# Kernel tuning notes

Hardware: AMD Instinct MI355X
Metric: run time of the kernel (lower is better)

## Reference

```python
import jax, jax.numpy as jnp
import numpy as np

B, H, NQ, NK, D = 2, 16, 4096, 4096, 64


def _attn_with_lse(q, k, v, scale):
    # q: [B,H,p,d], k: [B,H,s,d], v: [B,H,s,dv]
    s = jnp.einsum('bhqd,bhkd->bhqk', q, k) * scale
    lse = jax.nn.logsumexp(s, axis=-1, keepdims=True)  # [B,H,p,1]
    p = jnp.exp(s - lse)
    o = jnp.einsum('bhqk,bhkd->bhqd', p, v)
    return o, lse


def setup_inputs() -> dict:
    key = jax.random.key(0)
    k1, k2, k3 = jax.random.split(key, 3)
    return {
        'query': jax.random.normal(k1, (B, H, NQ, D), dtype=jnp.float32),
        'key': jax.random.normal(k2, (B, H, NK, D), dtype=jnp.float32),
        'value': jax.random.normal(k3, (B, H, NK, D), dtype=jnp.float32),
        'n_query_groups': 4,
        'n_key_groups': 4,
    }


def reference(query, key, value, n_query_groups, n_key_groups):
    b, h, nq, d = query.shape
    nk = key.shape[2]
    m, n = int(n_query_groups), int(n_key_groups)
    scale = d ** (-0.5)
    pq, pk = nq // m, nk // n  # group sizes n_gp
    c0, c1 = m // 2, n // 2   # center groups c_gp

    # representative query/key blocks
    q_gp = query[:, :, c0 * pq:(c0 + 1) * pq, :]              # [B,H,pq,d]
    k_gp = key[:, :, c1 * pk:(c1 + 1) * pk, :]                # [B,H,pk,d]
    # value chunks concatenated on feature dim (zero-padding of q/k in the
    # original leaves the dot products unchanged, so we skip it)
    v_gp = value.reshape(b, h, n, pk, d).transpose(0, 1, 3, 2, 4).reshape(b, h, pk, n * d)
    attn_gp, lse_gp = _attn_with_lse(q_gp, k_gp, v_gp, scale)  # [B,H,pq,n*d], [B,H,pq,1]

    # sample one key per key group (torch uses random.randint; fixed to 0 here)
    k_picked = 0
    k_sample = key[:, :, k_picked::pk, :]                      # [B,H,n,d]
    w = jnp.einsum('bhqd,bhnd->bhqn', query, k_sample)         # [B,H,nq,n]
    w_gps = w.reshape(b, h, m, pq, n)
    norm_gps = jnp.linalg.norm(w_gps, axis=-2)                 # [B,H,m,n]
    s_gps = norm_gps / norm_gps[:, :, c0, c1][:, :, None, None]

    v_sum = value.reshape(b, h, n, pk, d).sum(axis=3)          # [B,H,n,d]
    om = jnp.maximum(1.0 - s_gps, 0.0)                         # clamp(1-s, min=0)
    num_part1 = om[:, :, :, :, None, None] * v_sum[:, :, None, :, None, :]  # [B,H,m,n,1,d]
    den_part1 = (om * pk)[:, :, :, :, None, None]              # [B,H,m,n,1,1]

    lse_exp = jnp.exp(lse_gp)                                  # [B,H,pq,1]
    unnorm = lse_exp * attn_gp                                 # [B,H,pq,n*d]
    attn_gps = unnorm.reshape(b, h, pq, n, d).transpose(0, 1, 3, 2, 4)  # [B,H,n,pq,d]
    num_part2 = s_gps[:, :, :, :, None, None] * attn_gps[:, :, None, :, :, :]  # [B,H,m,n,pq,d]
    den_part2 = s_gps[:, :, :, :, None, None] * lse_exp[:, :, None, None, :, :]  # [B,H,m,n,pq,1]

    num_agg = (num_part1 + num_part2).sum(axis=3)              # [B,H,m,pq,d]
    den_agg = (den_part1 + den_part2).sum(axis=3)              # [B,H,m,pq,1]

    attn = (num_agg / den_agg).reshape(b, h, nq, d)
    lse = jnp.log(den_agg).reshape(b, h, nq, 1)
    return attn, lse
```

## Files before the change

kernel.cpp:

```cpp
#include <hip/hip_runtime.h>
#include <hip/hip_bf16.h>


#define BH_TOT 32
#define SEQ    4096
#define DIM    64
#define PQ     1024

#define QB_OFF 34816u
#define KB_OFF (QB_OFF + 4u*1024u*1024u)
#define VB_OFF (KB_OFF + 4u*1024u*1024u)
#define WS_NEED (VB_OFF + 16u*1024u*1024u)

#define QSCALE 0.1803368801111204f

typedef __attribute__((ext_vector_type(8))) short bf16x8;
typedef __attribute__((ext_vector_type(4))) short bf16x4;
typedef __attribute__((ext_vector_type(4))) float f32x4;
typedef __attribute__((ext_vector_type(4))) _Float16 f16x4;
typedef __attribute__((ext_vector_type(8))) _Float16 f16x8;

__device__ __forceinline__ short f2bf(float x) {
    unsigned u = __float_as_uint(x);
    u = u + 0x7fffu + ((u >> 16) & 1u);
    return (short)(u >> 16);
}
__device__ __forceinline__ float bf2f(unsigned short h) {
    return __uint_as_float(((unsigned)h) << 16);
}

__global__ __launch_bounds__(256) void mega_prep(
    const float* __restrict__ query, const float* __restrict__ key,
    const float* __restrict__ value, float* __restrict__ ws,
    char* __restrict__ wsb)
{
    __shared__ union {
        struct { float ksm[4][64]; float wsum[4][16]; } n;
        struct { float Ls[64][68]; float ps[4][64]; } v;
    } sm;
    const int t = threadIdx.x;
    const int bid = blockIdx.x;

    if (bid < 512) {
        const int bh = bid >> 4, gi = (bid >> 2) & 3, chunk = bid & 3;
        sm.n.ksm[t >> 6][t & 63] =
            key[((size_t)bh * SEQ + (size_t)(t >> 6) * PQ) * DIM + (t & 63)];
        __syncthreads();
        const int wv = t >> 6, lane = t & 63, c = lane & 15, hi = lane >> 4;
        bf16x8 bb0, bb1;
#pragma unroll
        for (int j = 0; j < 8; ++j) {
            bb0[j] = (c < 4) ? f2bf(sm.n.ksm[c][hi * 8 + j]) : (short)0;
            bb1[j] = (c < 4) ? f2bf(sm.n.ksm[c][32 + hi * 8 + j]) : (short)0;
        }
        float acc0 = 0.f, acc1 = 0.f, acc2 = 0.f, acc3 = 0.f;
        const float* qbase = query +
            ((size_t)bh * SEQ + (size_t)gi * PQ + (size_t)chunk * 256) * DIM;
#pragma unroll
        for (int it = 0; it < 4; ++it) {
            const int row = (wv * 4 + it) * 16 + c;
            const float* qp = qbase + (size_t)row * 64 + hi * 8;
            float4 a0 = *(const float4*)qp;
            float4 a1 = *(const float4*)(qp + 4);
            float4 a2 = *(const float4*)(qp + 32);
            float4 a3 = *(const float4*)(qp + 36);
            bf16x8 qa0, qa1;
            qa0[0] = f2bf(a0.x); qa0[1] = f2bf(a0.y); qa0[2] = f2bf(a0.z); qa0[3] = f2bf(a0.w);
            qa0[4] = f2bf(a1.x); qa0[5] = f2bf(a1.y); qa0[6] = f2bf(a1.z); qa0[7] = f2bf(a1.w);
            qa1[0] = f2bf(a2.x); qa1[1] = f2bf(a2.y); qa1[2] = f2bf(a2.z); qa1[3] = f2bf(a2.w);
            qa1[4] = f2bf(a3.x); qa1[5] = f2bf(a3.y); qa1[6] = f2bf(a3.z); qa1[7] = f2bf(a3.w);
            f32x4 s = (f32x4){0.f, 0.f, 0.f, 0.f};
            s = __builtin_amdgcn_mfma_f32_16x16x32_bf16(qa0, bb0, s, 0, 0, 0);
            s = __builtin_amdgcn_mfma_f32_16x16x32_bf16(qa1, bb1, s, 0, 0, 0);
            acc0 += s[0] * s[0]; acc1 += s[1] * s[1];
            acc2 += s[2] * s[2]; acc3 += s[3] * s[3];
        }
        float asum = acc0 + acc1 + acc2 + acc3;
        asum += __shfl_xor(asum, 16);
        asum += __shfl_xor(asum, 32);
        if (lane < 16) sm.n.wsum[wv][lane] = asum;
        __syncthreads();
        if (t < 4)
            atomicAdd(&ws[bh * 16 + gi * 4 + t],
                      sm.n.wsum[0][t] + sm.n.wsum[1][t] + sm.n.wsum[2][t] + sm.n.wsum[3][t]);
    } else if (bid < 2560) {
        const int blk = bid - 512;
        const int bh = blk >> 6, gj = (blk >> 4) & 3, kc = blk & 15;
        const float* src = value + ((size_t)bh * SEQ + gj * PQ + kc * 64) * DIM;
#pragma unroll
        for (int i = 0; i < 4; ++i) {
            const int u = t + i * 256;
            const int row = u >> 4, c4 = (u & 15) * 4;
            *(float4*)&sm.v.Ls[row][c4] = *(const float4*)(src + row * 64 + c4);
        }
        __syncthreads();
        {
            const int d = t & 63, rg = t >> 6;
            float s = 0.f;
#pragma unroll
            for (int i = 0; i < 16; ++i) s += sm.v.Ls[rg * 16 + i][d];
            sm.v.ps[rg][d] = s;
        }
        __syncthreads();
        if (t < 64) {
            float tot = sm.v.ps[0][t] + sm.v.ps[1][t] + sm.v.ps[2][t] + sm.v.ps[3][t];
            atomicAdd(&ws[512 + bh * 256 + gj * 64 + t], tot);
        }
#pragma unroll
        for (int i = 0; i < 2; ++i) {
            const int sid = t + i * 256;
            const int pl = sid >> 8, dt = (sid >> 6) & 3, lane = sid & 63;
            const int c = lane & 15, hi = lane >> 4;
            f16x8 h;
#pragma unroll
            for (int j = 0; j < 8; ++j)
                h[j] = (_Float16)sm.v.Ls[pl * 32 + hi * 8 + j][dt * 16 + c];
            const size_t off = ((((size_t)(bh * 4 + gj) * 32 + kc * 2 + pl) * 4 + dt) * 64 + lane) * 16;
            *(f16x8*)(wsb + VB_OFF + off) = h;
        }
    } else if (bid < 3072) {
        const int qb = bid - 2560;
        const int bh = qb >> 4, qt = qb & 15;
#pragma unroll
        for (int i = 0; i < 2; ++i) {
            const int sid = t + i * 256;
            const int mt = sid >> 7, kh = (sid >> 6) & 1, lane = sid & 63;
            const int c = lane & 15, hi = lane >> 4;
            const float* p = query + ((size_t)bh * SEQ + 2048 + qt * 64 + mt * 16 + c) * DIM
                             + kh * 32 + hi * 8;
            float4 a = *(const float4*)p, b = *(const float4*)(p + 4);
            bf16x8 h;
            h[0] = f2bf(a.x * QSCALE); h[1] = f2bf(a.y * QSCALE);
            h[2] = f2bf(a.z * QSCALE); h[3] = f2bf(a.w * QSCALE);
            h[4] = f2bf(b.x * QSCALE); h[5] = f2bf(b.y * QSCALE);
            h[6] = f2bf(b.z * QSCALE); h[7] = f2bf(b.w * QSCALE);
            const size_t fidx = ((size_t)(bh * 16 + qt) * 4 + mt) * 2 + kh;
            *(bf16x8*)(wsb + QB_OFF + fidx * 1024 + lane * 16) = h;
        }
    } else {
        const int b2 = bid - 3072;
        const int bh = b2 >> 4, kc = b2 & 15;
#pragma unroll
        for (int i = 0; i < 2; ++i) {
            const int sid = t + i * 256;
            const int kh = sid >> 8, nt = (sid >> 6) & 3, lane = sid & 63;
            const int c = lane & 15, hi = lane >> 4;
            const float* p = key + ((size_t)bh * SEQ + 2048 + kc * 64 + nt * 16 + c) * DIM
                             + kh * 32 + hi * 8;
            float4 a = *(const float4*)p, b = *(const float4*)(p + 4);
            bf16x8 h;
            h[0] = f2bf(a.x); h[1] = f2bf(a.y); h[2] = f2bf(a.z); h[3] = f2bf(a.w);
            h[4] = f2bf(b.x); h[5] = f2bf(b.y); h[6] = f2bf(b.z); h[7] = f2bf(b.w);
            const size_t fidx = ((size_t)(bh * 16 + kc) * 2 + kh) * 4 + nt;
            *(bf16x8*)(wsb + KB_OFF + fidx * 1024 + lane * 16) = h;
        }
    }
}

__global__ __launch_bounds__(256, 4) void kattn4(
    const char* __restrict__ wsb, float* __restrict__ out)
{
    __shared__ union {
        _Float16 Pf[2][2][2][512];
        float Uf[32][257];
    } lds;
    __shared__ float Llds[32];

    const int blk = blockIdx.x;
    const int slot = blk >> 3;
    const int bh = (blk & 7) * 4 + (slot >> 5);
    const int qt = slot & 31;
    const int t = threadIdx.x;
    const int w = t >> 6, lane = t & 63;
    const int c = lane & 15, hi = lane >> 4;

    bf16x8 aq[2][2];
#pragma unroll
    for (int qt2 = 0; qt2 < 2; ++qt2) {
        const int s = qt * 2 + qt2;
        const size_t fr = ((size_t)(bh * 16 + (s >> 2)) * 4 + (s & 3)) * 2;
        aq[qt2][0] = *(const bf16x8*)(wsb + QB_OFF + fr * 1024 + lane * 16);
        aq[qt2][1] = *(const bf16x8*)(wsb + QB_OFF + (fr + 1) * 1024 + lane * 16);
    }
    const char* kb = wsb + KB_OFF + ((size_t)(bh * 16) * 8) * 1024 + (size_t)w * 1024 + lane * 16;
    const char* vb = wsb + VB_OFF + ((size_t)(bh * 4 + w) * 128) * 1024 + lane * 16;

    f32x4 Uacc[2][4];
#pragma unroll
    for (int mt = 0; mt < 2; ++mt)
#pragma unroll
        for (int dt = 0; dt < 4; ++dt)
            Uacc[mt][dt] = (f32x4){0.f, 0.f, 0.f, 0.f};
    f32x4 Lacc[2];
    Lacc[0] = (f32x4){0.f, 0.f, 0.f, 0.f};
    Lacc[1] = (f32x4){0.f, 0.f, 0.f, 0.f};
    f16x8 kOnes;
#pragma unroll
    for (int j = 0; j < 8; ++j) kOnes[j] = (_Float16)1.f;

    const int k0 = w * 16 + hi * 4;
    const int pspan = k0 >> 5;
    const int pidx = (c + 16 * ((k0 & 31) >> 3)) * 8 + (k0 & 7);

    bf16x8 bk0 = *(const bf16x8*)(kb);
    bf16x8 bk1 = *(const bf16x8*)(kb + 4096);

    for (int kc = 0; kc < 16; ++kc) {
        const int buf = kc & 1;
        const char* vcb = vb + (size_t)kc * 8192;
        f16x8 vf[8];
#pragma unroll
        for (int u = 0; u < 8; ++u) vf[u] = *(const f16x8*)(vcb + u * 1024);
        f32x4 sacc[2];
        __builtin_amdgcn_s_setprio(1);
#pragma unroll
        for (int qt2 = 0; qt2 < 2; ++qt2) {
            f32x4 s = (f32x4){0.f, 0.f, 0.f, 0.f};
            s = __builtin_amdgcn_mfma_f32_16x16x32_bf16(bk0, aq[qt2][0], s, 0, 0, 0);
            s = __builtin_amdgcn_mfma_f32_16x16x32_bf16(bk1, aq[qt2][1], s, 0, 0, 0);
            sacc[qt2] = s;
        }
        __builtin_amdgcn_s_setprio(0);
        if (kc < 15) {
            bk0 = *(const bf16x8*)(kb + (size_t)(kc + 1) * 8192);
            bk1 = *(const bf16x8*)(kb + (size_t)(kc + 1) * 8192 + 4096);
        }
#pragma unroll
        for (int qt2 = 0; qt2 < 2; ++qt2) {
            f16x4 ph;
#pragma unroll
            for (int r = 0; r < 4; ++r)
                ph[r] = (_Float16)__builtin_amdgcn_exp2f(sacc[qt2][r]);
            *(f16x4*)&lds.Pf[buf][qt2][pspan][pidx] = ph;
        }
        asm volatile("s_waitcnt lgkmcnt(0)" ::: "memory");
        __builtin_amdgcn_s_barrier();
        f16x8 ap[2][2];
#pragma unroll
        for (int mt = 0; mt < 2; ++mt)
#pragma unroll
            for (int sp = 0; sp < 2; ++sp)
                ap[mt][sp] = *(const f16x8*)&lds.Pf[buf][mt][sp][lane * 8];
        __builtin_amdgcn_s_setprio(1);
#pragma unroll
        for (int mt = 0; mt < 2; ++mt) {
#pragma unroll
            for (int sp = 0; sp < 2; ++sp) {
                Uacc[mt][0] = __builtin_amdgcn_mfma_f32_16x16x32_f16(ap[mt][sp], vf[sp * 4 + 0], Uacc[mt][0], 0, 0, 0);
                Uacc[mt][1] = __builtin_amdgcn_mfma_f32_16x16x32_f16(ap[mt][sp], vf[sp * 4 + 1], Uacc[mt][1], 0, 0, 0);
                Uacc[mt][2] = __builtin_amdgcn_mfma_f32_16x16x32_f16(ap[mt][sp], vf[sp * 4 + 2], Uacc[mt][2], 0, 0, 0);
                Uacc[mt][3] = __builtin_amdgcn_mfma_f32_16x16x32_f16(ap[mt][sp], vf[sp * 4 + 3], Uacc[mt][3], 0, 0, 0);
                Lacc[mt]    = __builtin_amdgcn_mfma_f32_16x16x32_f16(ap[mt][sp], kOnes, Lacc[mt], 0, 0, 0);
            }
        }
        __builtin_amdgcn_s_setprio(0);
    }

    __syncthreads();
#pragma unroll
    for (int mt = 0; mt < 2; ++mt)
#pragma unroll
        for (int dt = 0; dt < 4; ++dt)
#pragma unroll
            for (int r = 0; r < 4; ++r)
                lds.Uf[mt * 16 + hi * 4 + r][w * 64 + dt * 16 + c] = Uacc[mt][dt][r];
    if (w == 0 && c == 0) {
#pragma unroll
        for (int mt = 0; mt < 2; ++mt)
#pragma unroll
            for (int r = 0; r < 4; ++r)
                Llds[mt * 16 + hi * 4 + r] = Lacc[mt][r];
    }
    __syncthreads();

    const float* wsf = (const float*)wsb;
    const float* nsq = wsf + (size_t)bh * 16;
    const float* vsw = wsf + 512 + (size_t)bh * 256;
    const int dd = t & 63, rq = t >> 6;
    float sg[4][4], ssum[4], omp[4], ov[4];
    const float inv22 = 1.0f / nsq[10];
#pragma unroll
    for (int gi = 0; gi < 4; ++gi) {
        float ss = 0.f, os = 0.f, ovv = 0.f;
#pragma unroll
        for (int gj = 0; gj < 4; ++gj) {
            float sgv = sqrtf(nsq[gi * 4 + gj] * inv22);
            sg[gi][gj] = sgv;
            ss += sgv;
            float om = fmaxf(1.0f - sgv, 0.0f);
            os += om;
            ovv += om * vsw[gj * 64 + dd];
        }
        ssum[gi] = ss; omp[gi] = os * 1024.0f; ov[gi] = ovv;
    }
    const size_t base = (size_t)bh * SEQ * DIM;
    float* attn_out = out + base;
    float* lse_out = out + (size_t)BH_TOT * SEQ * DIM + (size_t)bh * SEQ;
    for (int k = 0; k < 8; ++k) {
        const int r = k * 4 + rq;
        const float u0 = lds.Uf[r][dd];
        const float u1 = lds.Uf[r][64 + dd];
        const float u2 = lds.Uf[r][128 + dd];
        const float u3 = lds.Uf[r][192 + dd];
        const float Lr = Llds[r];
        const int orow = qt * 32 + r;
#pragma unroll
        for (int gi = 0; gi < 4; ++gi) {
            float num = ov[gi] + sg[gi][0] * u0 + sg[gi][1] * u1 + sg[gi][2] * u2 + sg[gi][3] * u3;
            float den = omp[gi] + ssum[gi] * Lr;
            attn_out[(size_t)(gi * 1024 + orow) * 64 + dd] = num * __builtin_amdgcn_rcpf(den);
            if (dd == gi) lse_out[gi * 1024 + orow] = __logf(den);
        }
    }
}

__global__ __launch_bounds__(256) void prep_norm2(
    const float* __restrict__ query, const float* __restrict__ key,
    float* __restrict__ ws)
{
    __shared__ float ksm[4][64];
    __shared__ float wsum[4][16];
    const int t = threadIdx.x;
    const int bh = blockIdx.x >> 2, gi = blockIdx.x & 3;
    if (t < 64) ws[512 + blockIdx.x * 64 + t] = 0.f;
    ksm[t >> 6][t & 63] = key[((size_t)bh * SEQ + (size_t)(t >> 6) * PQ) * DIM + (t & 63)];
    __syncthreads();
    const int wv = t >> 6, lane = t & 63, c = lane & 15, hi = lane >> 4;
    bf16x8 bb0, bb1;
#pragma unroll
    for (int j = 0; j < 8; ++j) {
        bb0[j] = (c < 4) ? f2bf(ksm[c][hi * 8 + j]) : (short)0;
        bb1[j] = (c < 4) ? f2bf(ksm[c][32 + hi * 8 + j]) : (short)0;
    }
    float acc0 = 0.f, acc1 = 0.f, acc2 = 0.f, acc3 = 0.f;
    const float* qbase = query + ((size_t)bh * SEQ + (size_t)gi * PQ) * DIM;
    for (int it = 0; it < 16; ++it) {
        const int row = (wv * 16 + it) * 16 + c;
        const float* qp = qbase + (size_t)row * 64 + hi * 8;
        float4 a0 = *(const float4*)qp;
        float4 a1 = *(const float4*)(qp + 4);
        float4 a2 = *(const float4*)(qp + 32);
        float4 a3 = *(const float4*)(qp + 36);
        bf16x8 qa0, qa1;
        qa0[0] = f2bf(a0.x); qa0[1] = f2bf(a0.y); qa0[2] = f2bf(a0.z); qa0[3] = f2bf(a0.w);
        qa0[4] = f2bf(a1.x); qa0[5] = f2bf(a1.y); qa0[6] = f2bf(a1.z); qa0[7] = f2bf(a1.w);
        qa1[0] = f2bf(a2.x); qa1[1] = f2bf(a2.y); qa1[2] = f2bf(a2.z); qa1[3] = f2bf(a2.w);
        qa1[4] = f2bf(a3.x); qa1[5] = f2bf(a3.y); qa1[6] = f2bf(a3.z); qa1[7] = f2bf(a3.w);
        f32x4 s = (f32x4){0.f, 0.f, 0.f, 0.f};
        s = __builtin_amdgcn_mfma_f32_16x16x32_bf16(qa0, bb0, s, 0, 0, 0);
        s = __builtin_amdgcn_mfma_f32_16x16x32_bf16(qa1, bb1, s, 0, 0, 0);
        acc0 += s[0] * s[0]; acc1 += s[1] * s[1];
        acc2 += s[2] * s[2]; acc3 += s[3] * s[3];
    }
    float asum = acc0 + acc1 + acc2 + acc3;
    asum += __shfl_xor(asum, 16);
    asum += __shfl_xor(asum, 32);
    if (lane < 16) wsum[wv][lane] = asum;
    __syncthreads();
    if (t < 4) ws[bh * 16 + gi * 4 + t] = wsum[0][t] + wsum[1][t] + wsum[2][t] + wsum[3][t];
}

__global__ __launch_bounds__(256) void prep_vsum(
    const float* __restrict__ value, float* __restrict__ ws)
{
    __shared__ float part[16][16][4];
    const int t = threadIdx.x;
    const int bh = blockIdx.x >> 2, gj = blockIdx.x & 3;
    const float4* vv = (const float4*)(value + ((size_t)bh * SEQ + (size_t)gj * PQ) * DIM);
    const int c4 = t & 15, rg = t >> 4;
    float a0 = 0.f, a1 = 0.f, a2 = 0.f, a3 = 0.f;
    for (int r = rg; r < 1024; r += 16) {
        float4 x = vv[r * 16 + c4];
        a0 += x.x; a1 += x.y; a2 += x.z; a3 += x.w;
    }
    part[rg][c4][0] = a0; part[rg][c4][1] = a1;
    part[rg][c4][2] = a2; part[rg][c4][3] = a3;
    __syncthreads();
    if (t < 64) {
        const int cc = t >> 2, comp = t & 3;
        float s = 0.f;
#pragma unroll
        for (int g = 0; g < 16; ++g) s += part[g][cc][comp];
        ws[512 + bh * 256 + gj * 64 + cc * 4 + comp] = s;
    }
}

__global__ __launch_bounds__(256, 2) void kattn_fallback(
    const float* __restrict__ query, const float* __restrict__ key,
    const float* __restrict__ value, const float* __restrict__ ws,
    float* __restrict__ out)
{
    __shared__ union {
        struct { short Q[64][72]; short K[64][72]; short P[64][72]; } s;
        unsigned short U[64][264];
    } lds;
    __shared__ float Llds[64];
    const int blk = blockIdx.x;
    const int bh = blk >> 4, qt = blk & 15;
    const int t = threadIdx.x;
    const int w = t >> 6, lane = t & 63;
    const int c = lane & 15, hi = lane >> 4;
    const size_t base = (size_t)bh * SEQ * DIM;
    {
        const float* qp = query + base + (size_t)(2048 + qt * 64) * DIM;
#pragma unroll
        for (int k2 = 0; k2 < 4; ++k2) {
            int u = t + k2 * 256;
            int row = u >> 4, ci = (u & 15) * 4;
            float4 qv = *(const float4*)(qp + row * 64 + ci);
            bf16x4 h;
            h[0] = f2bf(qv.x); h[1] = f2bf(qv.y); h[2] = f2bf(qv.z); h[3] = f2bf(qv.w);
            *(bf16x4*)&lds.s.Q[row][ci] = h;
        }
    }
    __syncthreads();
    bf16x8 aq0 = *(const bf16x8*)&lds.s.Q[w * 16 + c][hi * 8];
    bf16x8 aq1 = *(const bf16x8*)&lds.s.Q[w * 16 + c][32 + hi * 8];
    f32x4 Uacc[4][4];
#pragma unroll
    for (int mt = 0; mt < 4; ++mt)
#pragma unroll
        for (int nt = 0; nt < 4; ++nt)
            Uacc[mt][nt] = (f32x4){0.f, 0.f, 0.f, 0.f};
    float Lacc[4] = {0.f, 0.f, 0.f, 0.f};
    const float* kp = key + base + (size_t)2048 * DIM;
    const float* vgrp = value + base + (size_t)w * PQ * DIM;
    for (int kc = 0; kc < 16; ++kc) {
        {
            const float* kcp = kp + (size_t)kc * 64 * DIM;
#pragma unroll
            for (int k2 = 0; k2 < 4; ++k2) {
                int u = t + k2 * 256;
                int row = u >> 4, ci = (u & 15) * 4;
                float4 kv = *(const float4*)(kcp + row * 64 + ci);
                bf16x4 h;
                h[0] = f2bf(kv.x); h[1] = f2bf(kv.y); h[2] = f2bf(kv.z); h[3] = f2bf(kv.w);
                *(bf16x4*)&lds.s.K[row][ci] = h;
            }
        }
        __syncthreads();
        f32x4 sacc[4];
#pragma unroll
        for (int nt = 0; nt < 4; ++nt) sacc[nt] = (f32x4){0.f, 0.f, 0.f, 0.f};
#pragma unroll
        for (int nt = 0; nt < 4; ++nt) {
            bf16x8 bk = *(const bf16x8*)&lds.s.K[nt * 16 + c][hi * 8];
            sacc[nt] = __builtin_amdgcn_mfma_f32_16x16x32_bf16(aq0, bk, sacc[nt], 0, 0, 0);
        }
#pragma unroll
        for (int nt = 0; nt < 4; ++nt) {
            bf16x8 bk = *(const bf16x8*)&lds.s.K[nt * 16 + c][32 + hi * 8];
            sacc[nt] = __builtin_amdgcn_mfma_f32_16x16x32_bf16(aq1, bk, sacc[nt], 0, 0, 0);
        }
        float p[4][4];
#pragma unroll
        for (int nt = 0; nt < 4; ++nt)
#pragma unroll
            for (int r = 0; r < 4; ++r)
                p[nt][r] = __expf(sacc[nt][r] * 0.125f);
#pragma unroll
        for (int r = 0; r < 4; ++r) {
            float rs = p[0][r] + p[1][r] + p[2][r] + p[3][r];
            rs += __shfl_xor(rs, 1); rs += __shfl_xor(rs, 2);
            rs += __shfl_xor(rs, 4); rs += __shfl_xor(rs, 8);
            Lacc[r] += rs;
        }
#pragma unroll
        for (int nt = 0; nt < 4; ++nt)
#pragma unroll
            for (int r = 0; r < 4; ++r)
                lds.s.P[w * 16 + hi * 4 + r][nt * 16 + c] = (unsigned short)f2bf(p[nt][r]);
        __syncthreads();
        bf16x8 ap2[4][2];
#pragma unroll
        for (int mt = 0; mt < 4; ++mt) {
            ap2[mt][0] = *(const bf16x8*)&lds.s.P[mt * 16 + c][hi * 8];
            ap2[mt][1] = *(const bf16x8*)&lds.s.P[mt * 16 + c][32 + hi * 8];
        }
        const float* vp = vgrp + (size_t)kc * 64 * DIM;
#pragma unroll
        for (int kt = 0; kt < 2; ++kt) {
#pragma unroll
            for (int nt = 0; nt < 4; ++nt) {
                const float* vpp = vp + (kt * 32 + hi * 8) * 64 + nt * 16 + c;
                bf16x8 bv;
#pragma unroll
                for (int j = 0; j < 8; ++j) bv[j] = f2bf(vpp[j * 64]);
#pragma unroll
                for (int mt = 0; mt < 4; ++mt)
                    Uacc[mt][nt] = __builtin_amdgcn_mfma_f32_16x16x32_bf16(ap2[mt][kt], bv, Uacc[mt][nt], 0, 0, 0);
            }
        }
        __syncthreads();
    }
#pragma unroll
    for (int mt = 0; mt < 4; ++mt)
#pragma unroll
        for (int nt = 0; nt < 4; ++nt)
#pragma unroll
            for (int r = 0; r < 4; ++r)
                lds.U[mt * 16 + hi * 4 + r][w * 64 + nt * 16 + c] =
                    (unsigned short)f2bf(Uacc[mt][nt][r]);
    if (c == 0) {
#pragma unroll
        for (int r = 0; r < 4; ++r) Llds[w * 16 + hi * 4 + r] = Lacc[r];
    }
    __syncthreads();
    const float* nsq = ws + bh * 16;
    const float* vsw = ws + 512 + bh * 256;
    const int dd = t & 63, rq = t >> 6;
    float sg[4][4], ssum[4], omp[4], ov[4];
    const float inv22 = 1.0f / nsq[10];
#pragma unroll
    for (int gi = 0; gi < 4; ++gi) {
        float ss = 0.f, os = 0.f, ovv = 0.f;
#pragma unroll
        for (int gj = 0; gj < 4; ++gj) {
            float sgv = sqrtf(nsq[gi * 4 + gj] * inv22);
            sg[gi][gj] = sgv;
            ss += sgv;
            float om = fmaxf(1.0f - sgv, 0.0f);
            os += om;
            ovv += om * vsw[gj * 64 + dd];
        }
        ssum[gi] = ss; omp[gi] = os * 1024.0f; ov[gi] = ovv;
    }
    float* attn_out = out + base;
    float* lse_out = out + (size_t)BH_TOT * SEQ * DIM + (size_t)bh * SEQ;
    for (int k = 0; k < 16; ++k) {
        const int r = k * 4 + rq;
        const float u0 = bf2f(lds.U[r][dd]);
        const float u1 = bf2f(lds.U[r][64 + dd]);
        const float u2 = bf2f(lds.U[r][128 + dd]);
        const float u3 = bf2f(lds.U[r][192 + dd]);
        const float Lr = Llds[r];
        const int orow = qt * 64 + r;
#pragma unroll
        for (int gi = 0; gi < 4; ++gi) {
            float num = ov[gi] + sg[gi][0] * u0 + sg[gi][1] * u1 + sg[gi][2] * u2 + sg[gi][3] * u3;
            float den = omp[gi] + ssum[gi] * Lr;
            attn_out[(size_t)(gi * 1024 + orow) * 64 + dd] = num / den;
            if (dd == gi) lse_out[gi * 1024 + orow] = __logf(den);
        }
    }
}

extern "C" void kernel_launch(void* const* d_in, const int* in_sizes, int n_in,
                              void* d_out, int out_size, void* d_ws, size_t ws_size,
                              hipStream_t stream)
{
    (void)in_sizes; (void)n_in; (void)out_size;
    const float* query = (const float*)d_in[0];
    const float* key   = (const float*)d_in[1];
    const float* value = (const float*)d_in[2];
    float* ws   = (float*)d_ws;
    char*  wsb  = (char*)d_ws;
    float* outp = (float*)d_out;

    if (ws_size >= WS_NEED) {
        (void)hipMemsetAsync(d_ws, 0, QB_OFF, stream);
        mega_prep<<<3584, 256, 0, stream>>>(query, key, value, ws, wsb);
        kattn4<<<1024, 256, 0, stream>>>(wsb, outp);
    } else {
        prep_norm2<<<128, 256, 0, stream>>>(query, key, ws);
        prep_vsum<<<128, 256, 0, stream>>>(value, ws);
        kattn_fallback<<<512, 256, 0, stream>>>(query, key, value, ws, outp);
    }
}
```

Before: 170.8 us.

## Double query rows per attention block and compute prep norms with FP32 dot products

Each attention block now handles 64 query rows instead of 32, so every K/V fragment it loads feeds twice as many MFMAs. Launch bounds drop to 2 blocks per CU and the grid halves. The epilogue now stages U through LDS in 16-row slices to keep LDS usage down, at the cost of extra barriers. The query-norm prep path is also changed from bf16 MFMA to plain FP32 per-thread dot products with wave shuffles and direct atomics, trading matrix-unit work for scalar FMAs and more atomics.

```diff
diff --git a/kernel.cpp b/kernel.cpp
--- a/kernel.cpp
+++ b/kernel.cpp
@@ -35,7 +35,7 @@
     char* __restrict__ wsb)
 {
     __shared__ union {
-        struct { float ksm[4][64]; float wsum[4][16]; } n;
+        struct { float ksm[4][64]; } n;
         struct { float Ls[64][68]; float ps[4][64]; } v;
     } sm;
     const int t = threadIdx.x;
@@ -46,43 +46,36 @@
         sm.n.ksm[t >> 6][t & 63] =
             key[((size_t)bh * SEQ + (size_t)(t >> 6) * PQ) * DIM + (t & 63)];
         __syncthreads();
-        const int wv = t >> 6, lane = t & 63, c = lane & 15, hi = lane >> 4;
-        bf16x8 bb0, bb1;
-#pragma unroll
-        for (int j = 0; j < 8; ++j) {
-            bb0[j] = (c < 4) ? f2bf(sm.n.ksm[c][hi * 8 + j]) : (short)0;
-            bb1[j] = (c < 4) ? f2bf(sm.n.ksm[c][32 + hi * 8 + j]) : (short)0;
-        }
-        float acc0 = 0.f, acc1 = 0.f, acc2 = 0.f, acc3 = 0.f;
-        const float* qbase = query +
-            ((size_t)bh * SEQ + (size_t)gi * PQ + (size_t)chunk * 256) * DIM;
-#pragma unroll
-        for (int it = 0; it < 4; ++it) {
-            const int row = (wv * 4 + it) * 16 + c;
-            const float* qp = qbase + (size_t)row * 64 + hi * 8;
-            float4 a0 = *(const float4*)qp;
-            float4 a1 = *(const float4*)(qp + 4);
-            float4 a2 = *(const float4*)(qp + 32);
-            float4 a3 = *(const float4*)(qp + 36);
-            bf16x8 qa0, qa1;
-            qa0[0] = f2bf(a0.x); qa0[1] = f2bf(a0.y); qa0[2] = f2bf(a0.z); qa0[3] = f2bf(a0.w);
-            qa0[4] = f2bf(a1.x); qa0[5] = f2bf(a1.y); qa0[6] = f2bf(a1.z); qa0[7] = f2bf(a1.w);
-            qa1[0] = f2bf(a2.x); qa1[1] = f2bf(a2.y); qa1[2] = f2bf(a2.z); qa1[3] = f2bf(a2.w);
-            qa1[4] = f2bf(a3.x); qa1[5] = f2bf(a3.y); qa1[6] = f2bf(a3.z); qa1[7] = f2bf(a3.w);
-            f32x4 s = (f32x4){0.f, 0.f, 0.f, 0.f};
-            s = __builtin_amdgcn_mfma_f32_16x16x32_bf16(qa0, bb0, s, 0, 0, 0);
-            s = __builtin_amdgcn_mfma_f32_16x16x32_bf16(qa1, bb1, s, 0, 0, 0);
-            acc0 += s[0] * s[0]; acc1 += s[1] * s[1];
-            acc2 += s[2] * s[2]; acc3 += s[3] * s[3];
-        }
-        float asum = acc0 + acc1 + acc2 + acc3;
-        asum += __shfl_xor(asum, 16);
-        asum += __shfl_xor(asum, 32);
-        if (lane < 16) sm.n.wsum[wv][lane] = asum;
-        __syncthreads();
-        if (t < 4)
-            atomicAdd(&ws[bh * 16 + gi * 4 + t],
-                      sm.n.wsum[0][t] + sm.n.wsum[1][t] + sm.n.wsum[2][t] + sm.n.wsum[3][t]);
+        const int lane = t & 63;
+        const float* qp = query +
+            ((size_t)bh * SEQ + (size_t)gi * PQ + (size_t)chunk * 256 + t) * DIM;
+        float d0 = 0.f, d1 = 0.f, d2 = 0.f, d3 = 0.f;
+#pragma unroll
+        for (int j = 0; j < 16; ++j) {
+            float4 x = *(const float4*)(qp + j * 4);
+            const float* k0 = &sm.n.ksm[0][j * 4];
+            const float* k1 = &sm.n.ksm[1][j * 4];
+            const float* k2 = &sm.n.ksm[2][j * 4];
+            const float* k3 = &sm.n.ksm[3][j * 4];
+            d0 += x.x * k0[0] + x.y * k0[1] + x.z * k0[2] + x.w * k0[3];
+            d1 += x.x * k1[0] + x.y * k1[1] + x.z * k1[2] + x.w * k1[3];
+            d2 += x.x * k2[0] + x.y * k2[1] + x.z * k2[2] + x.w * k2[3];
+            d3 += x.x * k3[0] + x.y * k3[1] + x.z * k3[2] + x.w * k3[3];
+        }
+        float s0 = d0 * d0, s1 = d1 * d1, s2 = d2 * d2, s3 = d3 * d3;
+#pragma unroll
+        for (int off = 1; off < 64; off <<= 1) {
+            s0 += __shfl_xor(s0, off);
+            s1 += __shfl_xor(s1, off);
+            s2 += __shfl_xor(s2, off);
+            s3 += __shfl_xor(s3, off);
+        }
+        if (lane == 0) {
+            atomicAdd(&ws[bh * 16 + gi * 4 + 0], s0);
+            atomicAdd(&ws[bh * 16 + gi * 4 + 1], s1);
+            atomicAdd(&ws[bh * 16 + gi * 4 + 2], s2);
+            atomicAdd(&ws[bh * 16 + gi * 4 + 3], s3);
+        }
     } else if (bid < 2560) {
         const int blk = bid - 512;
         const int bh = blk >> 6, gj = (blk >> 4) & 3, kc = blk & 15;
@@ -157,43 +150,42 @@
     }
 }
 
-__global__ __launch_bounds__(256, 4) void kattn4(
+__global__ __launch_bounds__(256, 2) void kattn4(
     const char* __restrict__ wsb, float* __restrict__ out)
 {
     __shared__ union {
-        _Float16 Pf[2][2][2][512];
-        float Uf[32][257];
+        _Float16 Pf[2][4][2][512];
+        float Uf[16][257];
     } lds;
-    __shared__ float Llds[32];
+    __shared__ float Llds[64];
 
     const int blk = blockIdx.x;
     const int slot = blk >> 3;
-    const int bh = (blk & 7) * 4 + (slot >> 5);
-    const int qt = slot & 31;
+    const int bh = (blk & 7) * 4 + (slot >> 4);
+    const int qt = slot & 15;
     const int t = threadIdx.x;
     const int w = t >> 6, lane = t & 63;
     const int c = lane & 15, hi = lane >> 4;
 
-    bf16x8 aq[2][2];
-#pragma unroll
-    for (int qt2 = 0; qt2 < 2; ++qt2) {
-        const int s = qt * 2 + qt2;
-        const size_t fr = ((size_t)(bh * 16 + (s >> 2)) * 4 + (s & 3)) * 2;
+    bf16x8 aq[4][2];
+#pragma unroll
+    for (int qt2 = 0; qt2 < 4; ++qt2) {
+        const size_t fr = (((size_t)bh * 16 + qt) * 4 + qt2) * 2;
         aq[qt2][0] = *(const bf16x8*)(wsb + QB_OFF + fr * 1024 + lane * 16);
         aq[qt2][1] = *(const bf16x8*)(wsb + QB_OFF + (fr + 1) * 1024 + lane * 16);
     }
     const char* kb = wsb + KB_OFF + ((size_t)(bh * 16) * 8) * 1024 + (size_t)w * 1024 + lane * 16;
     const char* vb = wsb + VB_OFF + ((size_t)(bh * 4 + w) * 128) * 1024 + lane * 16;
 
-    f32x4 Uacc[2][4];
-#pragma unroll
-    for (int mt = 0; mt < 2; ++mt)
+    f32x4 Uacc[4][4];
+#pragma unroll
+    for (int mt = 0; mt < 4; ++mt)
 #pragma unroll
         for (int dt = 0; dt < 4; ++dt)
             Uacc[mt][dt] = (f32x4){0.f, 0.f, 0.f, 0.f};
-    f32x4 Lacc[2];
-    Lacc[0] = (f32x4){0.f, 0.f, 0.f, 0.f};
-    Lacc[1] = (f32x4){0.f, 0.f, 0.f, 0.f};
+    f32x4 Lacc[4];
+#pragma unroll
+    for (int mt = 0; mt < 4; ++mt) Lacc[mt] = (f32x4){0.f, 0.f, 0.f, 0.f};
     f16x8 kOnes;
 #pragma unroll
     for (int j = 0; j < 8; ++j) kOnes[j] = (_Float16)1.f;
@@ -211,10 +203,10 @@
         f16x8 vf[8];
 #pragma unroll
         for (int u = 0; u < 8; ++u) vf[u] = *(const f16x8*)(vcb + u * 1024);
-        f32x4 sacc[2];
+        f32x4 sacc[4];
         __builtin_amdgcn_s_setprio(1);
 #pragma unroll
-        for (int qt2 = 0; qt2 < 2; ++qt2) {
+        for (int qt2 = 0; qt2 < 4; ++qt2) {
             f32x4 s = (f32x4){0.f, 0.f, 0.f, 0.f};
             s = __builtin_amdgcn_mfma_f32_16x16x32_bf16(bk0, aq[qt2][0], s, 0, 0, 0);
             s = __builtin_amdgcn_mfma_f32_16x16x32_bf16(bk1, aq[qt2][1], s, 0, 0, 0);
@@ -226,7 +218,7 @@
             bk1 = *(const bf16x8*)(kb + (size_t)(kc + 1) * 8192 + 4096);
         }
 #pragma unroll
-        for (int qt2 = 0; qt2 < 2; ++qt2) {
+        for (int qt2 = 0; qt2 < 4; ++qt2) {
             f16x4 ph;
 #pragma unroll
             for (int r = 0; r < 4; ++r)
@@ -235,15 +227,15 @@
         }
         asm volatile("s_waitcnt lgkmcnt(0)" ::: "memory");
         __builtin_amdgcn_s_barrier();
-        f16x8 ap[2][2];
-#pragma unroll
-        for (int mt = 0; mt < 2; ++mt)
+        f16x8 ap[4][2];
+#pragma unroll
+        for (int mt = 0; mt < 4; ++mt)
 #pragma unroll
             for (int sp = 0; sp < 2; ++sp)
                 ap[mt][sp] = *(const f16x8*)&lds.Pf[buf][mt][sp][lane * 8];
         __builtin_amdgcn_s_setprio(1);
 #pragma unroll
-        for (int mt = 0; mt < 2; ++mt) {
+        for (int mt = 0; mt < 4; ++mt) {
 #pragma unroll
             for (int sp = 0; sp < 2; ++sp) {
                 Uacc[mt][0] = __builtin_amdgcn_mfma_f32_16x16x32_f16(ap[mt][sp], vf[sp * 4 + 0], Uacc[mt][0], 0, 0, 0);
@@ -257,21 +249,13 @@
     }
 
     __syncthreads();
-#pragma unroll
-    for (int mt = 0; mt < 2; ++mt)
-#pragma unroll
-        for (int dt = 0; dt < 4; ++dt)
-#pragma unroll
-            for (int r = 0; r < 4; ++r)
-                lds.Uf[mt * 16 + hi * 4 + r][w * 64 + dt * 16 + c] = Uacc[mt][dt][r];
     if (w == 0 && c == 0) {
 #pragma unroll
-        for (int mt = 0; mt < 2; ++mt)
+        for (int mt = 0; mt < 4; ++mt)
 #pragma unroll
             for (int r = 0; r < 4; ++r)
                 Llds[mt * 16 + hi * 4 + r] = Lacc[mt][r];
     }
-    __syncthreads();
 
     const float* wsf = (const float*)wsb;
     const float* nsq = wsf + (size_t)bh * 16;
@@ -296,21 +280,33 @@
     const size_t base = (size_t)bh * SEQ * DIM;
     float* attn_out = out + base;
     float* lse_out = out + (size_t)BH_TOT * SEQ * DIM + (size_t)bh * SEQ;
-    for (int k = 0; k < 8; ++k) {
-        const int r = k * 4 + rq;
-        const float u0 = lds.Uf[r][dd];
-        const float u1 = lds.Uf[r][64 + dd];
-        const float u2 = lds.Uf[r][128 + dd];
-        const float u3 = lds.Uf[r][192 + dd];
-        const float Lr = Llds[r];
-        const int orow = qt * 32 + r;
-#pragma unroll
-        for (int gi = 0; gi < 4; ++gi) {
-            float num = ov[gi] + sg[gi][0] * u0 + sg[gi][1] * u1 + sg[gi][2] * u2 + sg[gi][3] * u3;
-            float den = omp[gi] + ssum[gi] * Lr;
-            attn_out[(size_t)(gi * 1024 + orow) * 64 + dd] = num * __builtin_amdgcn_rcpf(den);
-            if (dd == gi) lse_out[gi * 1024 + orow] = __logf(den);
-        }
+
+#pragma unroll
+    for (int mt = 0; mt < 4; ++mt) {
+#pragma unroll
+        for (int dt = 0; dt < 4; ++dt)
+#pragma unroll
+            for (int r = 0; r < 4; ++r)
+                lds.Uf[hi * 4 + r][w * 64 + dt * 16 + c] = Uacc[mt][dt][r];
+        __syncthreads();
+#pragma unroll
+        for (int k = 0; k < 4; ++k) {
+            const int r = k * 4 + rq;
+            const float u0 = lds.Uf[r][dd];
+            const float u1 = lds.Uf[r][64 + dd];
+            const float u2 = lds.Uf[r][128 + dd];
+            const float u3 = lds.Uf[r][192 + dd];
+            const float Lr = Llds[mt * 16 + r];
+            const int orow = qt * 64 + mt * 16 + r;
+#pragma unroll
+            for (int gi = 0; gi < 4; ++gi) {
+                float num = ov[gi] + sg[gi][0] * u0 + sg[gi][1] * u1 + sg[gi][2] * u2 + sg[gi][3] * u3;
+                float den = omp[gi] + ssum[gi] * Lr;
+                attn_out[(size_t)(gi * 1024 + orow) * 64 + dd] = num * __builtin_amdgcn_rcpf(den);
+                if (dd == gi) lse_out[gi * 1024 + orow] = __logf(den);
+            }
+        }
+        __syncthreads();
     }
 }
 
@@ -560,7 +556,7 @@
     if (ws_size >= WS_NEED) {
         (void)hipMemsetAsync(d_ws, 0, QB_OFF, stream);
         mega_prep<<<3584, 256, 0, stream>>>(query, key, value, ws, wsb);
-        kattn4<<<1024, 256, 0, stream>>>(wsb, outp);
+        kattn4<<<512, 256, 0, stream>>>(wsb, outp);
     } else {
         prep_norm2<<<128, 256, 0, stream>>>(query, key, ws);
         prep_vsum<<<128, 256, 0, stream>>>(value, ws);
```

New measurement: 175.9 us. 1.03x slower.

## Software-pipeline QK and PV MFMAs across chunks and shrink epilogue LDS buffer

Applied to the files above, without the earlier changes.

Restructures the main loop into a prologue, steady state and epilogue. Each iteration issues the S=QK MFMAs for the next chunk alongside the PV MFMAs of the previous chunk, so the exp and LDS write of P overlap with matrix work, and the V/K global loads are issued after the MFMAs. The epilogue writes the U accumulator to LDS in four 8-row slices instead of all 32 rows at once. This cuts the LDS union to roughly a quarter of its size so more blocks may fit per CU, at the cost of extra barriers in the epilogue.

```diff
diff --git a/kernel.cpp b/kernel.cpp
--- a/kernel.cpp
+++ b/kernel.cpp
@@ -162,7 +162,7 @@
 {
     __shared__ union {
         _Float16 Pf[2][2][2][512];
-        float Uf[32][257];
+        float Uf[8][257];
     } lds;
     __shared__ float Llds[32];
 
@@ -205,14 +205,8 @@
     bf16x8 bk0 = *(const bf16x8*)(kb);
     bf16x8 bk1 = *(const bf16x8*)(kb + 4096);
 
-    for (int kc = 0; kc < 16; ++kc) {
-        const int buf = kc & 1;
-        const char* vcb = vb + (size_t)kc * 8192;
-        f16x8 vf[8];
-#pragma unroll
-        for (int u = 0; u < 8; ++u) vf[u] = *(const f16x8*)(vcb + u * 1024);
+    {
         f32x4 sacc[2];
-        __builtin_amdgcn_s_setprio(1);
 #pragma unroll
         for (int qt2 = 0; qt2 < 2; ++qt2) {
             f32x4 s = (f32x4){0.f, 0.f, 0.f, 0.f};
@@ -220,28 +214,40 @@
             s = __builtin_amdgcn_mfma_f32_16x16x32_bf16(bk1, aq[qt2][1], s, 0, 0, 0);
             sacc[qt2] = s;
         }
-        __builtin_amdgcn_s_setprio(0);
-        if (kc < 15) {
-            bk0 = *(const bf16x8*)(kb + (size_t)(kc + 1) * 8192);
-            bk1 = *(const bf16x8*)(kb + (size_t)(kc + 1) * 8192 + 4096);
-        }
+        bk0 = *(const bf16x8*)(kb + 8192);
+        bk1 = *(const bf16x8*)(kb + 8192 + 4096);
 #pragma unroll
         for (int qt2 = 0; qt2 < 2; ++qt2) {
             f16x4 ph;
 #pragma unroll
             for (int r = 0; r < 4; ++r)
                 ph[r] = (_Float16)__builtin_amdgcn_exp2f(sacc[qt2][r]);
-            *(f16x4*)&lds.Pf[buf][qt2][pspan][pidx] = ph;
-        }
-        asm volatile("s_waitcnt lgkmcnt(0)" ::: "memory");
-        __builtin_amdgcn_s_barrier();
+            *(f16x4*)&lds.Pf[0][qt2][pspan][pidx] = ph;
+        }
+    }
+    f16x8 vf[8];
+#pragma unroll
+    for (int u = 0; u < 8; ++u) vf[u] = *(const f16x8*)(vb + u * 1024);
+    asm volatile("s_waitcnt lgkmcnt(0)" ::: "memory");
+    __builtin_amdgcn_s_barrier();
+
+    for (int kc = 1; kc < 16; ++kc) {
+        const int cb = (kc - 1) & 1, pb = kc & 1;
         f16x8 ap[2][2];
 #pragma unroll
         for (int mt = 0; mt < 2; ++mt)
 #pragma unroll
             for (int sp = 0; sp < 2; ++sp)
-                ap[mt][sp] = *(const f16x8*)&lds.Pf[buf][mt][sp][lane * 8];
+                ap[mt][sp] = *(const f16x8*)&lds.Pf[cb][mt][sp][lane * 8];
+        f32x4 sacc[2];
         __builtin_amdgcn_s_setprio(1);
+#pragma unroll
+        for (int qt2 = 0; qt2 < 2; ++qt2) {
+            f32x4 s = (f32x4){0.f, 0.f, 0.f, 0.f};
+            s = __builtin_amdgcn_mfma_f32_16x16x32_bf16(bk0, aq[qt2][0], s, 0, 0, 0);
+            s = __builtin_amdgcn_mfma_f32_16x16x32_bf16(bk1, aq[qt2][1], s, 0, 0, 0);
+            sacc[qt2] = s;
+        }
 #pragma unroll
         for (int mt = 0; mt < 2; ++mt) {
 #pragma unroll
@@ -254,16 +260,47 @@
             }
         }
         __builtin_amdgcn_s_setprio(0);
+        const char* vcb = vb + (size_t)kc * 8192;
+#pragma unroll
+        for (int u = 0; u < 8; ++u) vf[u] = *(const f16x8*)(vcb + u * 1024);
+        if (kc < 15) {
+            bk0 = *(const bf16x8*)(kb + (size_t)(kc + 1) * 8192);
+            bk1 = *(const bf16x8*)(kb + (size_t)(kc + 1) * 8192 + 4096);
+        }
+#pragma unroll
+        for (int qt2 = 0; qt2 < 2; ++qt2) {
+            f16x4 ph;
+#pragma unroll
+            for (int r = 0; r < 4; ++r)
+                ph[r] = (_Float16)__builtin_amdgcn_exp2f(sacc[qt2][r]);
+            *(f16x4*)&lds.Pf[pb][qt2][pspan][pidx] = ph;
+        }
+        asm volatile("s_waitcnt lgkmcnt(0)" ::: "memory");
+        __builtin_amdgcn_s_barrier();
+    }
+    {
+        f16x8 ap[2][2];
+#pragma unroll
+        for (int mt = 0; mt < 2; ++mt)
+#pragma unroll
+            for (int sp = 0; sp < 2; ++sp)
+                ap[mt][sp] = *(const f16x8*)&lds.Pf[1][mt][sp][lane * 8];
+        __builtin_amdgcn_s_setprio(1);
+#pragma unroll
+        for (int mt = 0; mt < 2; ++mt) {
+#pragma unroll
+            for (int sp = 0; sp < 2; ++sp) {
+                Uacc[mt][0] = __builtin_amdgcn_mfma_f32_16x16x32_f16(ap[mt][sp], vf[sp * 4 + 0], Uacc[mt][0], 0, 0, 0);
+                Uacc[mt][1] = __builtin_amdgcn_mfma_f32_16x16x32_f16(ap[mt][sp], vf[sp * 4 + 1], Uacc[mt][1], 0, 0, 0);
+                Uacc[mt][2] = __builtin_amdgcn_mfma_f32_16x16x32_f16(ap[mt][sp], vf[sp * 4 + 2], Uacc[mt][2], 0, 0, 0);
+                Uacc[mt][3] = __builtin_amdgcn_mfma_f32_16x16x32_f16(ap[mt][sp], vf[sp * 4 + 3], Uacc[mt][3], 0, 0, 0);
+                Lacc[mt]    = __builtin_amdgcn_mfma_f32_16x16x32_f16(ap[mt][sp], kOnes, Lacc[mt], 0, 0, 0);
+            }
+        }
+        __builtin_amdgcn_s_setprio(0);
     }
 
     __syncthreads();
-#pragma unroll
-    for (int mt = 0; mt < 2; ++mt)
-#pragma unroll
-        for (int dt = 0; dt < 4; ++dt)
-#pragma unroll
-            for (int r = 0; r < 4; ++r)
-                lds.Uf[mt * 16 + hi * 4 + r][w * 64 + dt * 16 + c] = Uacc[mt][dt][r];
     if (w == 0 && c == 0) {
 #pragma unroll
         for (int mt = 0; mt < 2; ++mt)
@@ -271,7 +308,6 @@
             for (int r = 0; r < 4; ++r)
                 Llds[mt * 16 + hi * 4 + r] = Lacc[mt][r];
     }
-    __syncthreads();
 
     const float* wsf = (const float*)wsb;
     const float* nsq = wsf + (size_t)bh * 16;
@@ -296,20 +332,38 @@
     const size_t base = (size_t)bh * SEQ * DIM;
     float* attn_out = out + base;
     float* lse_out = out + (size_t)BH_TOT * SEQ * DIM + (size_t)bh * SEQ;
-    for (int k = 0; k < 8; ++k) {
-        const int r = k * 4 + rq;
-        const float u0 = lds.Uf[r][dd];
-        const float u1 = lds.Uf[r][64 + dd];
-        const float u2 = lds.Uf[r][128 + dd];
-        const float u3 = lds.Uf[r][192 + dd];
-        const float Lr = Llds[r];
-        const int orow = qt * 32 + r;
-#pragma unroll
-        for (int gi = 0; gi < 4; ++gi) {
-            float num = ov[gi] + sg[gi][0] * u0 + sg[gi][1] * u1 + sg[gi][2] * u2 + sg[gi][3] * u3;
-            float den = omp[gi] + ssum[gi] * Lr;
-            attn_out[(size_t)(gi * 1024 + orow) * 64 + dd] = num * __builtin_amdgcn_rcpf(den);
-            if (dd == gi) lse_out[gi * 1024 + orow] = __logf(den);
+
+#pragma unroll
+    for (int mt = 0; mt < 2; ++mt) {
+#pragma unroll
+        for (int half = 0; half < 2; ++half) {
+            if ((hi >> 1) == half) {
+#pragma unroll
+                for (int dt = 0; dt < 4; ++dt)
+#pragma unroll
+                    for (int r = 0; r < 4; ++r)
+                        lds.Uf[(hi & 1) * 4 + r][w * 64 + dt * 16 + c] = Uacc[mt][dt][r];
+            }
+            __syncthreads();
+#pragma unroll
+            for (int k = 0; k < 2; ++k) {
+                const int rloc = k * 4 + rq;
+                const float u0 = lds.Uf[rloc][dd];
+                const float u1 = lds.Uf[rloc][64 + dd];
+                const float u2 = lds.Uf[rloc][128 + dd];
+                const float u3 = lds.Uf[rloc][192 + dd];
+                const int rrow = mt * 16 + half * 8 + rloc;
+                const float Lr = Llds[rrow];
+                const int orow = qt * 32 + rrow;
+#pragma unroll
+                for (int gi = 0; gi < 4; ++gi) {
+                    float num = ov[gi] + sg[gi][0] * u0 + sg[gi][1] * u1 + sg[gi][2] * u2 + sg[gi][3] * u3;
+                    float den = omp[gi] + ssum[gi] * Lr;
+                    attn_out[(size_t)(gi * 1024 + orow) * 64 + dd] = num * __builtin_amdgcn_rcpf(den);
+                    if (dd == gi) lse_out[gi * 1024 + orow] = __logf(den);
+                }
+            }
+            __syncthreads();
         }
     }
 }
```

Result: slower. 186.2 us (+9.0%).

## Keep P in registers and split keys across waves, reducing accumulators in LDS

Applied to the files above, without the earlier changes.

The attention kernel no longer passes the exponentiated scores through LDS with a per-iteration barrier. Each wave now owns a 16-key slice and feeds its P fragment straight from registers into 16x16x16 f16 MFMAs over all four value groups. The value layout in the prep kernel is changed to match. This removes the in-loop LDS round trip and barrier, at the cost of a 4x larger accumulator set (lower occupancy, launch bounds 4->2), more LDS, and a cross-wave reduction of U and L at the end.

```diff
diff --git a/kernel.cpp b/kernel.cpp
--- a/kernel.cpp
+++ b/kernel.cpp
@@ -107,16 +107,20 @@
             atomicAdd(&ws[512 + bh * 256 + gj * 64 + t], tot);
         }
 #pragma unroll
-        for (int i = 0; i < 2; ++i) {
+        for (int i = 0; i < 4; ++i) {
             const int sid = t + i * 256;
-            const int pl = sid >> 8, dt = (sid >> 6) & 3, lane = sid & 63;
+            const int kl = sid >> 8;
+            const int dt = (sid >> 6) & 3;
+            const int lane = sid & 63;
             const int c = lane & 15, hi = lane >> 4;
-            f16x8 h;
-#pragma unroll
-            for (int j = 0; j < 8; ++j)
-                h[j] = (_Float16)sm.v.Ls[pl * 32 + hi * 8 + j][dt * 16 + c];
-            const size_t off = ((((size_t)(bh * 4 + gj) * 32 + kc * 2 + pl) * 4 + dt) * 64 + lane) * 16;
-            *(f16x8*)(wsb + VB_OFF + off) = h;
+            f16x4 h;
+#pragma unroll
+            for (int j = 0; j < 4; ++j)
+                h[j] = (_Float16)sm.v.Ls[kl * 16 + hi * 4 + j][dt * 16 + c];
+            const size_t k16 = (size_t)kc * 4 + kl;
+            const size_t off = (((size_t)(bh * 4 + gj) * 64 + k16) * 4 + dt) * 512
+                               + (size_t)lane * 8;
+            *(f16x4*)(wsb + VB_OFF + off) = h;
         }
     } else if (bid < 3072) {
         const int qb = bid - 2560;
@@ -157,14 +161,12 @@
     }
 }
 
-__global__ __launch_bounds__(256, 4) void kattn4(
+__global__ __launch_bounds__(256, 2) void kattn4(
     const char* __restrict__ wsb, float* __restrict__ out)
 {
-    __shared__ union {
-        _Float16 Pf[2][2][2][512];
-        float Uf[32][257];
-    } lds;
-    __shared__ float Llds[32];
+    __shared__ float Uf[32][257];
+    __shared__ float Ug[32][257];
+    __shared__ float Lp[4][32];
 
     const int blk = blockIdx.x;
     const int slot = blk >> 3;
@@ -183,36 +185,37 @@
         aq[qt2][1] = *(const bf16x8*)(wsb + QB_OFF + (fr + 1) * 1024 + lane * 16);
     }
     const char* kb = wsb + KB_OFF + ((size_t)(bh * 16) * 8) * 1024 + (size_t)w * 1024 + lane * 16;
-    const char* vb = wsb + VB_OFF + ((size_t)(bh * 4 + w) * 128) * 1024 + lane * 16;
-
-    f32x4 Uacc[2][4];
-#pragma unroll
-    for (int mt = 0; mt < 2; ++mt)
-#pragma unroll
-        for (int dt = 0; dt < 4; ++dt)
-            Uacc[mt][dt] = (f32x4){0.f, 0.f, 0.f, 0.f};
+
+    f32x4 Uacc[2][4][4];
+#pragma unroll
+    for (int qt2 = 0; qt2 < 2; ++qt2)
+#pragma unroll
+        for (int gj = 0; gj < 4; ++gj)
+#pragma unroll
+            for (int dt = 0; dt < 4; ++dt)
+                Uacc[qt2][gj][dt] = (f32x4){0.f, 0.f, 0.f, 0.f};
     f32x4 Lacc[2];
     Lacc[0] = (f32x4){0.f, 0.f, 0.f, 0.f};
     Lacc[1] = (f32x4){0.f, 0.f, 0.f, 0.f};
-    f16x8 kOnes;
-#pragma unroll
-    for (int j = 0; j < 8; ++j) kOnes[j] = (_Float16)1.f;
-
-    const int k0 = w * 16 + hi * 4;
-    const int pspan = k0 >> 5;
-    const int pidx = (c + 16 * ((k0 & 31) >> 3)) * 8 + (k0 & 7);
+    f16x4 ones16;
+#pragma unroll
+    for (int j = 0; j < 4; ++j) ones16[j] = (_Float16)1.f;
 
     bf16x8 bk0 = *(const bf16x8*)(kb);
     bf16x8 bk1 = *(const bf16x8*)(kb + 4096);
 
     for (int kc = 0; kc < 16; ++kc) {
-        const int buf = kc & 1;
-        const char* vcb = vb + (size_t)kc * 8192;
-        f16x8 vf[8];
-#pragma unroll
-        for (int u = 0; u < 8; ++u) vf[u] = *(const f16x8*)(vcb + u * 1024);
+        f16x4 vf[4][4];
+        const size_t k16 = (size_t)kc * 4 + w;
+#pragma unroll
+        for (int gj = 0; gj < 4; ++gj) {
+            const char* vp = wsb + VB_OFF
+                + ((size_t)(bh * 4 + gj) * 64 + k16) * 2048 + (size_t)lane * 8;
+#pragma unroll
+            for (int dt = 0; dt < 4; ++dt)
+                vf[gj][dt] = *(const f16x4*)(vp + (size_t)dt * 512);
+        }
         f32x4 sacc[2];
-        __builtin_amdgcn_s_setprio(1);
 #pragma unroll
         for (int qt2 = 0; qt2 < 2; ++qt2) {
             f32x4 s = (f32x4){0.f, 0.f, 0.f, 0.f};
@@ -220,56 +223,70 @@
             s = __builtin_amdgcn_mfma_f32_16x16x32_bf16(bk1, aq[qt2][1], s, 0, 0, 0);
             sacc[qt2] = s;
         }
-        __builtin_amdgcn_s_setprio(0);
         if (kc < 15) {
             bk0 = *(const bf16x8*)(kb + (size_t)(kc + 1) * 8192);
             bk1 = *(const bf16x8*)(kb + (size_t)(kc + 1) * 8192 + 4096);
         }
+        f16x4 pa[2];
+#pragma unroll
+        for (int qt2 = 0; qt2 < 2; ++qt2)
+#pragma unroll
+            for (int r = 0; r < 4; ++r)
+                pa[qt2][r] = (_Float16)__builtin_amdgcn_exp2f(sacc[qt2][r]);
+        __builtin_amdgcn_s_setprio(1);
 #pragma unroll
         for (int qt2 = 0; qt2 < 2; ++qt2) {
-            f16x4 ph;
+#pragma unroll
+            for (int gj = 0; gj < 4; ++gj) {
+                Uacc[qt2][gj][0] = __builtin_amdgcn_mfma_f32_16x16x16f16(pa[qt2], vf[gj][0], Uacc[qt2][gj][0], 0, 0, 0);
+                Uacc[qt2][gj][1] = __builtin_amdgcn_mfma_f32_16x16x16f16(pa[qt2], vf[gj][1], Uacc[qt2][gj][1], 0, 0, 0);
+                Uacc[qt2][gj][2] = __builtin_amdgcn_mfma_f32_16x16x16f16(pa[qt2], vf[gj][2], Uacc[qt2][gj][2], 0, 0, 0);
+                Uacc[qt2][gj][3] = __builtin_amdgcn_mfma_f32_16x16x16f16(pa[qt2], vf[gj][3], Uacc[qt2][gj][3], 0, 0, 0);
+            }
+            Lacc[qt2] = __builtin_amdgcn_mfma_f32_16x16x16f16(pa[qt2], ones16, Lacc[qt2], 0, 0, 0);
+        }
+        __builtin_amdgcn_s_setprio(0);
+    }
+
+    if (c == 0) {
+#pragma unroll
+        for (int qt2 = 0; qt2 < 2; ++qt2)
 #pragma unroll
             for (int r = 0; r < 4; ++r)
-                ph[r] = (_Float16)__builtin_amdgcn_exp2f(sacc[qt2][r]);
-            *(f16x4*)&lds.Pf[buf][qt2][pspan][pidx] = ph;
-        }
-        asm volatile("s_waitcnt lgkmcnt(0)" ::: "memory");
-        __builtin_amdgcn_s_barrier();
-        f16x8 ap[2][2];
-#pragma unroll
-        for (int mt = 0; mt < 2; ++mt)
-#pragma unroll
-            for (int sp = 0; sp < 2; ++sp)
-                ap[mt][sp] = *(const f16x8*)&lds.Pf[buf][mt][sp][lane * 8];
-        __builtin_amdgcn_s_setprio(1);
-#pragma unroll
-        for (int mt = 0; mt < 2; ++mt) {
-#pragma unroll
-            for (int sp = 0; sp < 2; ++sp) {
-                Uacc[mt][0] = __builtin_amdgcn_mfma_f32_16x16x32_f16(ap[mt][sp], vf[sp * 4 + 0], Uacc[mt][0], 0, 0, 0);
-                Uacc[mt][1] = __builtin_amdgcn_mfma_f32_16x16x32_f16(ap[mt][sp], vf[sp * 4 + 1], Uacc[mt][1], 0, 0, 0);
-                Uacc[mt][2] = __builtin_amdgcn_mfma_f32_16x16x32_f16(ap[mt][sp], vf[sp * 4 + 2], Uacc[mt][2], 0, 0, 0);
-                Uacc[mt][3] = __builtin_amdgcn_mfma_f32_16x16x32_f16(ap[mt][sp], vf[sp * 4 + 3], Uacc[mt][3], 0, 0, 0);
-                Lacc[mt]    = __builtin_amdgcn_mfma_f32_16x16x32_f16(ap[mt][sp], kOnes, Lacc[mt], 0, 0, 0);
-            }
-        }
-        __builtin_amdgcn_s_setprio(0);
-    }
-
-    __syncthreads();
-#pragma unroll
-    for (int mt = 0; mt < 2; ++mt)
-#pragma unroll
-        for (int dt = 0; dt < 4; ++dt)
-#pragma unroll
-            for (int r = 0; r < 4; ++r)
-                lds.Uf[mt * 16 + hi * 4 + r][w * 64 + dt * 16 + c] = Uacc[mt][dt][r];
-    if (w == 0 && c == 0) {
-#pragma unroll
-        for (int mt = 0; mt < 2; ++mt)
-#pragma unroll
-            for (int r = 0; r < 4; ++r)
-                Llds[mt * 16 + hi * 4 + r] = Lacc[mt][r];
+                Lp[w][qt2 * 16 + hi * 4 + r] = Lacc[qt2][r];
+    }
+    if (w < 2) {
+        float (*dst)[257] = (w == 0) ? Uf : Ug;
+#pragma unroll
+        for (int qt2 = 0; qt2 < 2; ++qt2)
+#pragma unroll
+            for (int gj = 0; gj < 4; ++gj)
+#pragma unroll
+                for (int dt = 0; dt < 4; ++dt)
+#pragma unroll
+                    for (int r = 0; r < 4; ++r)
+                        dst[qt2 * 16 + hi * 4 + r][gj * 64 + dt * 16 + c] = Uacc[qt2][gj][dt][r];
+    }
+    __syncthreads();
+    if (w >= 2) {
+        float (*dst)[257] = (w == 2) ? Uf : Ug;
+#pragma unroll
+        for (int qt2 = 0; qt2 < 2; ++qt2)
+#pragma unroll
+            for (int gj = 0; gj < 4; ++gj)
+#pragma unroll
+                for (int dt = 0; dt < 4; ++dt)
+#pragma unroll
+                    for (int r = 0; r < 4; ++r)
+                        dst[qt2 * 16 + hi * 4 + r][gj * 64 + dt * 16 + c] += Uacc[qt2][gj][dt][r];
+    }
+    __syncthreads();
+#pragma unroll
+    for (int rr = 0; rr < 8; ++rr) {
+        const int row = w * 8 + rr;
+#pragma unroll
+        for (int col4 = 0; col4 < 4; ++col4)
+            Uf[row][col4 * 64 + lane] += Ug[row][col4 * 64 + lane];
     }
     __syncthreads();
 
@@ -298,11 +315,11 @@
     float* lse_out = out + (size_t)BH_TOT * SEQ * DIM + (size_t)bh * SEQ;
     for (int k = 0; k < 8; ++k) {
         const int r = k * 4 + rq;
-        const float u0 = lds.Uf[r][dd];
-        const float u1 = lds.Uf[r][64 + dd];
-        const float u2 = lds.Uf[r][128 + dd];
-        const float u3 = lds.Uf[r][192 + dd];
-        const float Lr = Llds[r];
+        const float u0 = Uf[r][dd];
+        const float u1 = Uf[r][64 + dd];
+        const float u2 = Uf[r][128 + dd];
+        const float u3 = Uf[r][192 + dd];
+        const float Lr = Lp[0][r] + Lp[1][r] + Lp[2][r] + Lp[3][r];
         const int orow = qt * 32 + r;
 #pragma unroll
         for (int gi = 0; gi < 4; ++gi) {
```

New measurement: 189.2 us. 10.8% more time.
